# Kernel optimization log

Measured on AMD Instinct MI355X. Metric: run time of the kernel, lower is better.

Reference implementation:

```python
import jax, jax.numpy as jnp
import numpy as np

N = 8192      # atoms
E = 4096      # edges (become transformer tokens)
E2 = 65536    # edges of second graph y
VOCAB = 119
DE = 200      # node_features == embedding_dim
D = 256
H = 8
L = 2
DFF = 2048


def _bn(x, g, b, eps=1e-6):
    m = x.mean(0)
    v = x.var(0)
    return (x - m) * jax.lax.rsqrt(v + eps) * g + b


def _ln(x, g, b, eps=1e-5):
    m = x.mean(-1, keepdims=True)
    v = ((x - m) ** 2).mean(-1, keepdims=True)
    return (x - m) * jax.lax.rsqrt(v + eps) * g + b


def _gcn(x, ei, W, b):
    # PyG GCNConv: add self loops, symmetric deg^-1/2 normalization
    n = x.shape[0]
    loop = jnp.arange(n)
    src = jnp.concatenate([ei[0], loop])
    dst = jnp.concatenate([ei[1], loop])
    deg = jax.ops.segment_sum(jnp.ones(src.shape[0], x.dtype), dst, num_segments=n)
    dinv = jnp.where(deg > 0, jax.lax.rsqrt(jnp.maximum(deg, 1e-12)), 0.0)
    msg = (x @ W)[src] * (dinv[src] * dinv[dst])[:, None]
    return jax.ops.segment_sum(msg, dst, num_segments=n) + b


def _mha(x, wi, bi, wo, bo):
    S, d = x.shape
    dh = d // H
    q, k, v = jnp.split(x @ wi + bi, 3, axis=1)
    q = q.reshape(S, H, dh)
    k = k.reshape(S, H, dh)
    v = v.reshape(S, H, dh)
    sc = jnp.einsum('qhd,khd->hqk', q, k) * (1.0 / np.sqrt(dh))
    a = jax.nn.softmax(sc, axis=-1)
    o = jnp.einsum('hqk,khd->qhd', a, v).reshape(S, d)
    return o @ wo + bo


def setup_inputs() -> dict:
    key = jax.random.key(0)
    ks = iter(jax.random.split(key, 64))
    nrm = lambda shape, s=0.05: jax.random.normal(next(ks), shape, jnp.float32) * s
    d = {}
    d['x'] = jax.random.randint(next(ks), (N,), 0, VOCAB)
    d['edge_index'] = jax.random.randint(next(ks), (2, E), 1, N + 1)  # 1-based, code subtracts 1
    d['pos'] = jax.random.normal(next(ks), (N, 3), jnp.float32)
    d['y'] = jax.random.randint(next(ks), (2, E2), 0, E)
    d['emb'] = nrm((VOCAB, DE), 1.0)
    d['fc1_w'] = nrm((1, DE))
    d['fc1_b'] = jnp.zeros((DE,), jnp.float32)
    d['bn4_g'] = jnp.ones((DE,), jnp.float32)
    d['bn4_b'] = jnp.zeros((DE,), jnp.float32)
    d['conv1_w'] = nrm((DE, D))
    d['conv1_b'] = jnp.zeros((D,), jnp.float32)
    d['conv2_w'] = nrm((D, D))
    d['conv2_b'] = jnp.zeros((D,), jnp.float32)
    for i in (1, 2, 3):
        d['bn%d_g' % i] = jnp.ones((D,), jnp.float32)
        d['bn%d_b' % i] = jnp.zeros((D,), jnp.float32)
    d['in_proj_w'] = nrm((L, D, 3 * D))
    d['in_proj_b'] = jnp.zeros((L, 3 * D), jnp.float32)
    d['out_proj_w'] = nrm((L, D, D))
    d['out_proj_b'] = jnp.zeros((L, D), jnp.float32)
    d['ln1_g'] = jnp.ones((L, D), jnp.float32)
    d['ln1_b'] = jnp.zeros((L, D), jnp.float32)
    d['ln2_g'] = jnp.ones((L, D), jnp.float32)
    d['ln2_b'] = jnp.zeros((L, D), jnp.float32)
    d['ff1_w'] = nrm((L, D, DFF))
    d['ff1_b'] = jnp.zeros((L, DFF), jnp.float32)
    d['ff2_w'] = nrm((L, DFF, D))
    d['ff2_b'] = jnp.zeros((L, D), jnp.float32)
    d['fc3_w'] = nrm((D, 1))
    d['fc3_b'] = jnp.zeros((1,), jnp.float32)
    d['fc4_w'] = nrm((D, 9))
    d['fc4_b'] = jnp.zeros((9,), jnp.float32)
    return d


def reference(x, edge_index, pos, y, emb, fc1_w, fc1_b, bn4_g, bn4_b,
              conv1_w, conv1_b, conv2_w, conv2_b,
              bn1_g, bn1_b, bn2_g, bn2_b, bn3_g, bn3_b,
              in_proj_w, in_proj_b, out_proj_w, out_proj_b,
              ln1_g, ln1_b, ln2_g, ln2_b, ff1_w, ff1_b, ff2_w, ff2_b,
              fc3_w, fc3_b, fc4_w, fc4_b):
    h = emb[x]                                   # [N, DE]
    ei = edge_index - 1
    row, col = ei[0], ei[1]
    ef = jnp.linalg.norm(pos[col] - pos[row], axis=1, keepdims=True)  # [E,1]
    ef = _bn(ef @ fc1_w + fc1_b, bn4_g, bn4_b)   # [E, DE]
    h = h[row] + h[col] + ef                     # [E, DE] edges -> tokens
    h = jax.nn.leaky_relu(_gcn(h, y, conv1_w, conv1_b))
    h = _bn(h, bn1_g, bn1_b)
    h = jax.nn.leaky_relu(h + _gcn(h, y, conv2_w, conv2_b))
    h = _bn(h, bn2_g, bn2_b)
    # post-norm TransformerEncoder (unbatched seq of length E), dropout=0
    for i in range(L):
        h = _ln(h + _mha(h, in_proj_w[i], in_proj_b[i], out_proj_w[i], out_proj_b[i]),
                ln1_g[i], ln1_b[i])
        ff = jax.nn.relu(h @ ff1_w[i] + ff1_b[i]) @ ff2_w[i] + ff2_b[i]
        h = _ln(h + ff, ln2_g[i], ln2_b[i])
    h = jax.nn.leaky_relu(h)
    h = _bn(h, bn3_g, bn3_b)
    sym_out = h @ fc3_w + fc3_b
    asym_out = h @ fc4_w + fc4_b
    return (sym_out, asym_out)
```

## Files before the change

### kernel.cpp

```cpp
#include <hip/hip_runtime.h>
#include <math.h>

#define ETOK 4096
#define NE2  65536
#define DEF  200
#define DM   256
#define NH   8
#define DH   32
#define DFFN 2048
#define NKS  8

#define QSCALE_LOG2E 0.25503474f

typedef __attribute__((ext_vector_type(8))) short bfrag8;
typedef __attribute__((ext_vector_type(4))) float f32x4;
typedef __attribute__((ext_vector_type(4))) short short4v;
typedef __attribute__((ext_vector_type(4))) unsigned int u32x4;

__device__ __forceinline__ unsigned short f2bf(float f) {
  union { float f; unsigned u; } v; v.f = f;
  unsigned u = v.u + 0x7fffu + ((v.u >> 16) & 1u);
  return (unsigned short)(u >> 16);
}
__device__ __forceinline__ float bf2f(unsigned short u) {
  union { unsigned u; float f; } v;
  v.u = ((unsigned)u) << 16;
  return v.f;
}
__device__ __forceinline__ unsigned cvt_pk_bf16(float lo, float hi) {
  unsigned r;
  asm("v_cvt_pk_bf16_f32 %0, %1, %2" : "=v"(r) : "v"(lo), "v"(hi));
  return r;
}

__device__ __forceinline__ float wave_sum(float v) {
#pragma unroll
  for (int off = 32; off > 0; off >>= 1) v += __shfl_xor(v, off);
  return v;
}
__device__ __forceinline__ float block_sum(float v, float* red) {
  v = wave_sum(v);
  int lane = threadIdx.x & 63, w = threadIdx.x >> 6;
  if (lane == 0) red[w] = v;
  __syncthreads();
  float t = red[0] + red[1] + red[2] + red[3];
  __syncthreads();
  return t;
}

__global__ void edge_deg_kernel(const int* __restrict__ ei, const float* __restrict__ pos,
                                float* __restrict__ ef0, float* __restrict__ stats,
                                const int* __restrict__ y, int* __restrict__ deg) {
  __shared__ float red[4];
  int e2 = blockIdx.x * 256 + threadIdx.x;
  atomicAdd(&deg[y[NE2 + e2]], 1);
  if (blockIdx.x < 16) {
    int e = blockIdx.x * 256 + threadIdx.x;
    int r = ei[e] - 1;
    int c = ei[ETOK + e] - 1;
    float dx = pos[c * 3 + 0] - pos[r * 3 + 0];
    float dy = pos[c * 3 + 1] - pos[r * 3 + 1];
    float dz = pos[c * 3 + 2] - pos[r * 3 + 2];
    float d = sqrtf(dx * dx + dy * dy + dz * dz);
    ef0[e] = d;
    float s = block_sum(d, red);
    float s2 = block_sum(d * d, red);
    if (threadIdx.x == 0) {
      atomicAdd(stats + 0, s);
      atomicAdd(stats + 1, s2);
    }
  }
}

__global__ void token_build_kernel(const int* __restrict__ x, const int* __restrict__ ei,
                                   const float* __restrict__ emb, const float* __restrict__ fc1_w,
                                   const float* __restrict__ bn4_g, const float* __restrict__ bn4_b,
                                   const float* __restrict__ ef0, const float* __restrict__ stats,
                                   unsigned short* __restrict__ tokbf) {
  int e = blockIdx.x;
  int j = threadIdx.x;
  float m = stats[0] * (1.0f / 4096.0f);
  float v = stats[1] * (1.0f / 4096.0f) - m * m;
  int xr = x[ei[e] - 1];
  int xc = x[ei[ETOK + e] - 1];
  float dd = ef0[e] - m;
  float val = 0.f;
  if (j < DEF) {
    float w = fc1_w[j];
    float s = w * rsqrtf(v * w * w + 1e-6f) * bn4_g[j];
    val = emb[(size_t)xr * DEF + j] + emb[(size_t)xc * DEF + j] + dd * s + bn4_b[j];
  }
  tokbf[(size_t)e * 256 + j] = f2bf(val);
}

__global__ void scan_kernel(const int* __restrict__ deg, int* __restrict__ off,
                            int* __restrict__ cursor, float* __restrict__ dinv) {
  __shared__ int part[256];
  int t = threadIdx.x;
  int v[16];
  int s = 0;
#pragma unroll
  for (int i = 0; i < 16; ++i) {
    v[i] = deg[t * 16 + i];
    s += v[i];
  }
  part[t] = s;
  __syncthreads();
  if (t == 0) {
    int a = 0;
#pragma unroll 1
    for (int i = 0; i < 256; ++i) {
      int tmp = part[i];
      part[i] = a;
      a += tmp;
    }
    off[4096] = a;
  }
  __syncthreads();
  int a = part[t];
#pragma unroll
  for (int i = 0; i < 16; ++i) {
    off[t * 16 + i] = a;
    cursor[t * 16 + i] = a;
    dinv[t * 16 + i] = rsqrtf((float)(v[i] + 1));
    a += v[i];
  }
}
__global__ void fill_kernel(const int* __restrict__ y, int* __restrict__ cursor,
                            int* __restrict__ srcl) {
  int e = blockIdx.x * 256 + threadIdx.x;
  int s = y[e];
  int d = y[NE2 + e];
  int slot = atomicAdd(&cursor[d], 1);
  srcl[slot] = s;
}

template <int RES, int ACT>
__global__ __launch_bounds__(256) void gather_kernel(const float* __restrict__ xw,
                                                     const int* __restrict__ off,
                                                     const int* __restrict__ srcl,
                                                     const float* __restrict__ dinv,
                                                     const float* __restrict__ bias,
                                                     const float* __restrict__ resid,
                                                     float* __restrict__ out) {
  __shared__ int slds[256];
  __shared__ float dlds[256];
  const int d = blockIdx.x;
  const int c = threadIdx.x;
  const int b0 = off[d], b1 = off[d + 1];
  const float dd = dinv[d];
  float acc = 0.f;
  for (int base = b0; base < b1; base += 256) {
    int n = min(256, b1 - base);
    __syncthreads();
    if (c < n) {
      int s = srcl[base + c];
      slds[c] = s;
      dlds[c] = dinv[s];
    }
    __syncthreads();
    for (int j = 0; j < n; ++j) {
      int s = slds[j];
      acc = fmaf(xw[(size_t)s * DM + c], dlds[j], acc);
    }
  }
  size_t idx = (size_t)d * DM + c;
  float v = bias[c] + xw[idx] * dd * dd + acc * dd;
  if (RES) v += resid[idx];
  if (ACT) v = v > 0.f ? v : 0.01f * v;
  out[idx] = v;
}

struct WEntry {
  const float* src;
  unsigned short* dst;
  int K, N, KP, tilesN, ntiles;
};
struct WPack {
  WEntry e[10];
};
__global__ __launch_bounds__(256) void wtrans_all_kernel(WPack p) {
  __shared__ float tl[32][33];
  int t = blockIdx.x;
  int i = 0;
  while (t >= p.e[i].ntiles) {
    t -= p.e[i].ntiles;
    ++i;
  }
  const WEntry w = p.e[i];
  int nb = (t % w.tilesN) * 32;
  int kb = (t / w.tilesN) * 32;
  int tx = threadIdx.x & 31, ty = threadIdx.x >> 5;
#pragma unroll
  for (int r = ty; r < 32; r += 8) {
    int k = kb + r, n = nb + tx;
    tl[r][tx] = (k < w.K && n < w.N) ? w.src[(size_t)k * w.N + n] : 0.f;
  }
  __syncthreads();
#pragma unroll
  for (int r = ty; r < 32; r += 8) {
    int n = nb + r, k = kb + tx;
    if (n < w.N) w.dst[(size_t)n * w.KP + k] = f2bf(tl[tx][r]);
  }
}

template <int BM, int BN, int OUTBF, int ACT, int QS, int VSPLIT>
__global__ __launch_bounds__(256) void mfma_gemm(const unsigned short* __restrict__ A,
                                                 const unsigned short* __restrict__ Bt,
                                                 const float* __restrict__ bias,
                                                 void* __restrict__ Cout, void* __restrict__ Cout2,
                                                 int M, int N, int K) {
  constexpr int BK = 64;
  constexpr int TM = BM / 32, TN = BN / 32;
  constexpr int ACH = BM / 32, BCH = BN / 32;
  __shared__ unsigned short Alds[BM * BK];
  __shared__ unsigned short Blds[BN * BK];
  const int tid = threadIdx.x;
  const int lane = tid & 63, wid = tid >> 6;
  const int g = lane >> 4, q = lane & 15;
  const int wr = wid >> 1, wc = wid & 1;
  const int m0 = blockIdx.y * BM, n0 = blockIdx.x * BN;

  f32x4 acc[TM][TN];
#pragma unroll
  for (int i = 0; i < TM; ++i)
#pragma unroll
    for (int j = 0; j < TN; ++j) acc[i][j] = (f32x4){0.f, 0.f, 0.f, 0.f};

  for (int k0 = 0; k0 < K; k0 += BK) {
    __syncthreads();
#pragma unroll
    for (int c = 0; c < ACH; ++c) {
      int chunk = wid * ACH + c;
      int row = chunk * 8 + (lane >> 3);
      int cb = ((lane & 7) * 16) ^ ((row & 7) << 4);
      const char* gp = (const char*)A + ((size_t)(m0 + row) * K + k0) * 2 + cb;
      __builtin_amdgcn_global_load_lds(
          (const __attribute__((address_space(1))) unsigned int*)gp,
          (__attribute__((address_space(3))) unsigned int*)(Alds + chunk * 512), 16, 0, 0);
    }
#pragma unroll
    for (int c = 0; c < BCH; ++c) {
      int chunk = wid * BCH + c;
      int row = chunk * 8 + (lane >> 3);
      int cb = ((lane & 7) * 16) ^ ((row & 7) << 4);
      const char* gp = (const char*)Bt + ((size_t)(n0 + row) * K + k0) * 2 + cb;
      __builtin_amdgcn_global_load_lds(
          (const __attribute__((address_space(1))) unsigned int*)gp,
          (__attribute__((address_space(3))) unsigned int*)(Blds + chunk * 512), 16, 0, 0);
    }
    __syncthreads();
#pragma unroll
    for (int ks = 0; ks < 2; ++ks) {
      bfrag8 af[TM], bfr[TN];
#pragma unroll
      for (int mi = 0; mi < TM; ++mi) {
        int row = wr * (BM / 2) + mi * 16 + q;
        int cb = (ks * 64 + g * 16) ^ ((row & 7) << 4);
        af[mi] = *(const bfrag8*)((const char*)Alds + row * 128 + cb);
      }
#pragma unroll
      for (int ni = 0; ni < TN; ++ni) {
        int row = wc * (BN / 2) + ni * 16 + q;
        int cb = (ks * 64 + g * 16) ^ ((row & 7) << 4);
        bfr[ni] = *(const bfrag8*)((const char*)Blds + row * 128 + cb);
      }
#pragma unroll
      for (int mi = 0; mi < TM; ++mi)
#pragma unroll
        for (int ni = 0; ni < TN; ++ni)
          acc[mi][ni] = __builtin_amdgcn_mfma_f32_16x16x32_bf16(af[mi], bfr[ni], acc[mi][ni], 0, 0, 0);
    }
  }
#pragma unroll
  for (int mi = 0; mi < TM; ++mi) {
    int row = m0 + wr * (BM / 2) + mi * 16 + g * 4;
#pragma unroll
    for (int ni = 0; ni < TN; ++ni) {
      int col = n0 + wc * (BN / 2) + ni * 16 + q;
      float bv = bias ? bias[col] : 0.f;
      if (VSPLIT && col >= 512) {
        short4v pkv;
#pragma unroll
        for (int r = 0; r < 4; ++r) pkv[r] = (short)f2bf(acc[mi][ni][r] + bv);
        *(short4v*)((unsigned short*)Cout2 + (size_t)(col - 512) * M + row) = pkv;
      } else {
#pragma unroll
        for (int r = 0; r < 4; ++r) {
          float v = acc[mi][ni][r] + bv;
          if (QS && col < DM) v *= QSCALE_LOG2E;
          if (ACT == 1) v = fmaxf(v, 0.f);
          if (OUTBF)
            ((unsigned short*)Cout)[(size_t)(row + r) * (VSPLIT ? 512 : N) + col] = f2bf(v);
          else
            ((float*)Cout)[(size_t)(row + r) * N + col] = v;
        }
      }
    }
  }
}

template <int LEAKY>
__global__ __launch_bounds__(256) void col_accum_kernel(const float* __restrict__ x,
                                                        float* __restrict__ colm,
                                                        float* __restrict__ colv) {
  int c = threadIdx.x;
  int r0 = blockIdx.x * 16;
  float s = 0.f, s2 = 0.f;
#pragma unroll
  for (int i = 0; i < 16; ++i) {
    float v = x[(size_t)(r0 + i) * DM + c];
    if (LEAKY) v = v > 0.f ? v : 0.01f * v;
    s += v;
    s2 += v * v;
  }
  atomicAdd(&colm[c], s);
  atomicAdd(&colv[c], s2);
}
template <int LEAKY>
__global__ void bn_apply_kernel(const float* __restrict__ x, const float* __restrict__ colm,
                                const float* __restrict__ colv, const float* __restrict__ g,
                                const float* __restrict__ b, float* __restrict__ outf,
                                unsigned short* __restrict__ outb, int C) {
  size_t i = (size_t)blockIdx.x * 256 + threadIdx.x;
  int c = (int)(i % C);
  float mean = colm[c] * (1.0f / 4096.0f);
  float var = colv[c] * (1.0f / 4096.0f) - mean * mean;
  float v0 = x[i];
  if (LEAKY) v0 = v0 > 0.f ? v0 : 0.01f * v0;
  float v = (v0 - mean) * rsqrtf(var + 1e-6f) * g[c] + b[c];
  outf[i] = v;
  if (outb) outb[i] = f2bf(v);
}

__global__ __launch_bounds__(256, 6) void attn_mfma_kernel(const unsigned short* __restrict__ qk,
                                                           const unsigned short* __restrict__ vt,
                                                           unsigned short* __restrict__ Opart,
                                                           float* __restrict__ Lpart) {
  const int h = blockIdx.y;
  const int qblk = blockIdx.x * 128;
  const int chunk = blockIdx.z;
  const int tid = threadIdx.x;
  const int wid = tid >> 6, lane = tid & 63;
  const int g = lane >> 4, q = lane & 15;

  __shared__ unsigned short Klds[64][40];
  __shared__ unsigned int Vtw[32][36];
  __shared__ unsigned short Plds[4][32][40];

  bfrag8 qfrag0, qfrag1;
  {
    const unsigned short* qp = qk + (size_t)(qblk + wid * 32 + q) * 512 + h * DH + g * 8;
    qfrag0 = *(const bfrag8*)qp;
    qfrag1 = *(const bfrag8*)(qp + 16 * 512);
  }
  bfrag8 ones;
#pragma unroll
  for (int i = 0; i < 8; ++i) ones[i] = (short)0x3F80;
  const f32x4 zero = {0.f, 0.f, 0.f, 0.f};

  const int skey = tid >> 2;
  const int sdb = (tid & 3) * 8;
  const int sd = tid >> 3;
  const int sk4 = (tid & 7) * 4;

  const int kbeg = chunk * (ETOK / NKS);
  const int NT = (ETOK / NKS) / 64;

  const unsigned short* kptr = qk + (size_t)(kbeg + skey) * 512 + DM + h * DH + sdb;
  const unsigned short* vptr = vt + (size_t)(h * DH + sd) * ETOK + kbeg + sk4 * 2;

  bfrag8 kreg = *(const bfrag8*)kptr;
  kptr += (size_t)64 * 512;
  u32x4 vreg = *(const u32x4*)vptr;
  vptr += 64;

  f32x4 o00 = zero, o01 = zero, o10 = zero, o11 = zero;
  f32x4 ol0 = zero, ol1 = zero;

  for (int t = 0; t < NT; ++t) {
    *(bfrag8*)&Klds[skey][sdb] = kreg;
    *(u32x4*)&Vtw[sd][sk4] = vreg;
    __syncthreads();
    if (t + 1 < NT) {
      kreg = *(const bfrag8*)kptr;
      kptr += (size_t)64 * 512;
      vreg = *(const u32x4*)vptr;
      vptr += 64;
    }

#pragma unroll
    for (int kg = 0; kg < 2; ++kg) {
      f32x4 s0a, s0b, s1a, s1b;
      __builtin_amdgcn_s_setprio(1);
      {
        bfrag8 kfa = *(const bfrag8*)&Klds[(2 * kg) * 16 + q][g * 8];
        bfrag8 kfb = *(const bfrag8*)&Klds[(2 * kg + 1) * 16 + q][g * 8];
        s0a = __builtin_amdgcn_mfma_f32_16x16x32_bf16(kfa, qfrag0, zero, 0, 0, 0);
        s1a = __builtin_amdgcn_mfma_f32_16x16x32_bf16(kfa, qfrag1, zero, 0, 0, 0);
        s0b = __builtin_amdgcn_mfma_f32_16x16x32_bf16(kfb, qfrag0, zero, 0, 0, 0);
        s1b = __builtin_amdgcn_mfma_f32_16x16x32_bf16(kfb, qfrag1, zero, 0, 0, 0);
      }
      __builtin_amdgcn_s_setprio(0);

      {
        uint2 w2;
        w2.x = cvt_pk_bf16(__builtin_exp2f(s0a[0]), __builtin_exp2f(s0a[1]));
        w2.y = cvt_pk_bf16(__builtin_exp2f(s0a[2]), __builtin_exp2f(s0a[3]));
        *(uint2*)&Plds[wid][q][g * 4] = w2;
        w2.x = cvt_pk_bf16(__builtin_exp2f(s0b[0]), __builtin_exp2f(s0b[1]));
        w2.y = cvt_pk_bf16(__builtin_exp2f(s0b[2]), __builtin_exp2f(s0b[3]));
        *(uint2*)&Plds[wid][q][16 + g * 4] = w2;
        w2.x = cvt_pk_bf16(__builtin_exp2f(s1a[0]), __builtin_exp2f(s1a[1]));
        w2.y = cvt_pk_bf16(__builtin_exp2f(s1a[2]), __builtin_exp2f(s1a[3]));
        *(uint2*)&Plds[wid][16 + q][g * 4] = w2;
        w2.x = cvt_pk_bf16(__builtin_exp2f(s1b[0]), __builtin_exp2f(s1b[1]));
        w2.y = cvt_pk_bf16(__builtin_exp2f(s1b[2]), __builtin_exp2f(s1b[3]));
        *(uint2*)&Plds[wid][16 + q][16 + g * 4] = w2;
      }

      __builtin_amdgcn_s_setprio(1);
      {
        bfrag8 pa0 = *(const bfrag8*)&Plds[wid][q][g * 8];
        bfrag8 pa1 = *(const bfrag8*)&Plds[wid][16 + q][g * 8];
        bfrag8 vb0 = *(const bfrag8*)&Vtw[q][kg * 16 + g * 4];
        bfrag8 vb1 = *(const bfrag8*)&Vtw[16 + q][kg * 16 + g * 4];
        o00 = __builtin_amdgcn_mfma_f32_16x16x32_bf16(pa0, vb0, o00, 0, 0, 0);
        o01 = __builtin_amdgcn_mfma_f32_16x16x32_bf16(pa0, vb1, o01, 0, 0, 0);
        o10 = __builtin_amdgcn_mfma_f32_16x16x32_bf16(pa1, vb0, o10, 0, 0, 0);
        o11 = __builtin_amdgcn_mfma_f32_16x16x32_bf16(pa1, vb1, o11, 0, 0, 0);
        ol0 = __builtin_amdgcn_mfma_f32_16x16x32_bf16(pa0, ones, ol0, 0, 0, 0);
        ol1 = __builtin_amdgcn_mfma_f32_16x16x32_bf16(pa1, ones, ol1, 0, 0, 0);
      }
      __builtin_amdgcn_s_setprio(0);
    }
    __syncthreads();
  }

#pragma unroll
  for (int r = 0; r < 4; ++r) {
    int row0 = qblk + wid * 32 + g * 4 + r;
    unsigned short* op0 = Opart + ((size_t)chunk * ETOK + row0) * DM + h * DH;
    op0[q] = f2bf(o00[r]);
    op0[16 + q] = f2bf(o01[r]);
    unsigned short* op1 = op0 + (size_t)16 * DM;
    op1[q] = f2bf(o10[r]);
    op1[16 + q] = f2bf(o11[r]);
  }
  if (q == 0) {
#pragma unroll
    for (int r = 0; r < 4; ++r) {
      int row = qblk + wid * 32 + g * 4 + r;
      Lpart[((size_t)chunk * ETOK + row) * NH + h] = ol0[r];
      Lpart[((size_t)chunk * ETOK + row + 16) * NH + h] = ol1[r];
    }
  }
}

__global__ __launch_bounds__(256) void attn_combine_kernel(const unsigned short* __restrict__ Opart,
                                                           const float* __restrict__ Lpart,
                                                           unsigned short* __restrict__ out) {
  __shared__ float ls[NKS][NH];
  const int row = blockIdx.x;
  const int c = threadIdx.x;
  if (c < NKS * NH) {
    ls[c >> 3][c & 7] = Lpart[((size_t)(c >> 3) * ETOK + row) * NH + (c & 7)];
  }
  __syncthreads();
  const int h = c >> 5;
  float lstar = 0.f, acc = 0.f;
#pragma unroll
  for (int ch = 0; ch < NKS; ++ch) {
    lstar += ls[ch][h];
    acc += bf2f(Opart[((size_t)ch * ETOK + row) * DM + c]);
  }
  out[(size_t)row * DM + c] = f2bf(acc / lstar);
}

__global__ void add_ln_kernel(const float* __restrict__ x, const float* __restrict__ r,
                              float* __restrict__ outf, unsigned short* __restrict__ outb,
                              const float* __restrict__ g, const float* __restrict__ b) {
  __shared__ float red[4];
  int row = blockIdx.x, t = threadIdx.x;
  size_t idx = (size_t)row * DM + t;
  float v = x[idx] + r[idx];
  float mean = block_sum(v, red) * (1.0f / 256.0f);
  float dv = v - mean;
  float var = block_sum(dv * dv, red) * (1.0f / 256.0f);
  float o = dv * rsqrtf(var + 1e-5f) * g[t] + b[t];
  outf[idx] = o;
  outb[idx] = f2bf(o);
}

__global__ void head_kernel(const float* __restrict__ h, const float* __restrict__ colm,
                            const float* __restrict__ colv, const float* __restrict__ bng,
                            const float* __restrict__ bnb, const float* __restrict__ fc3w,
                            const float* __restrict__ fc3b, const float* __restrict__ fc4w,
                            const float* __restrict__ fc4b, float* __restrict__ out) {
  int wave = threadIdx.x >> 6, lane = threadIdx.x & 63;
  int tok = blockIdx.x * 4 + wave;
  const float* hr = h + (size_t)tok * DM;
  float hv[4];
#pragma unroll
  for (int i = 0; i < 4; ++i) {
    int col = lane * 4 + i;
    float v = hr[col];
    v = v > 0.f ? v : 0.01f * v;
    float mean = colm[col] * (1.0f / 4096.0f);
    float var = colv[col] * (1.0f / 4096.0f) - mean * mean;
    hv[i] = (v - mean) * rsqrtf(var + 1e-6f) * bng[col] + bnb[col];
  }
  float acc = 0.f;
#pragma unroll
  for (int i = 0; i < 4; ++i) acc += hv[i] * fc3w[lane * 4 + i];
  acc = wave_sum(acc);
  if (lane == 0) out[tok] = acc + fc3b[0];
#pragma unroll
  for (int j = 0; j < 9; ++j) {
    float a = 0.f;
#pragma unroll
    for (int i = 0; i < 4; ++i) a += hv[i] * fc4w[(lane * 4 + i) * 9 + j];
    a = wave_sum(a);
    if (lane == 0) out[ETOK + (size_t)tok * 9 + j] = a + fc4b[j];
  }
}

extern "C" void kernel_launch(void* const* d_in, const int* in_sizes, int n_in,
                              void* d_out, int out_size, void* d_ws, size_t ws_size,
                              hipStream_t stream) {
  const int* x = (const int*)d_in[0];
  const int* edge_index = (const int*)d_in[1];
  const float* pos = (const float*)d_in[2];
  const int* y = (const int*)d_in[3];
  const float* emb = (const float*)d_in[4];
  const float* fc1_w = (const float*)d_in[5];
  const float* bn4_g = (const float*)d_in[7];
  const float* bn4_b = (const float*)d_in[8];
  const float* conv1_w = (const float*)d_in[9];
  const float* conv1_b = (const float*)d_in[10];
  const float* conv2_w = (const float*)d_in[11];
  const float* conv2_b = (const float*)d_in[12];
  const float* bn1_g = (const float*)d_in[13];
  const float* bn1_b = (const float*)d_in[14];
  const float* bn2_g = (const float*)d_in[15];
  const float* bn2_b = (const float*)d_in[16];
  const float* bn3_g = (const float*)d_in[17];
  const float* bn3_b = (const float*)d_in[18];
  const float* ipw = (const float*)d_in[19];
  const float* ipb = (const float*)d_in[20];
  const float* opw = (const float*)d_in[21];
  const float* opb = (const float*)d_in[22];
  const float* ln1_g = (const float*)d_in[23];
  const float* ln1_b = (const float*)d_in[24];
  const float* ln2_g = (const float*)d_in[25];
  const float* ln2_b = (const float*)d_in[26];
  const float* ff1w = (const float*)d_in[27];
  const float* ff1b = (const float*)d_in[28];
  const float* ff2w = (const float*)d_in[29];
  const float* ff2b = (const float*)d_in[30];
  const float* fc3w = (const float*)d_in[31];
  const float* fc3b = (const float*)d_in[32];
  const float* fc4w = (const float*)d_in[33];
  const float* fc4b = (const float*)d_in[34];
  float* outp = (float*)d_out;

  char* wsp = (char*)d_ws;
  auto alloc = [&](size_t bytes) {
    void* p = (void*)wsp;
    wsp += (bytes + 255) & ~(size_t)255;
    return p;
  };
  unsigned short* big_bf = (unsigned short*)alloc((size_t)ETOK * DFFN * 2);
  unsigned short* qk_bf = (unsigned short*)alloc((size_t)ETOK * 512 * 2);
  unsigned short* vt_bf = (unsigned short*)alloc((size_t)DM * ETOK * 2);
  unsigned short* attno = (unsigned short*)alloc((size_t)ETOK * DM * 2);
  unsigned short* h_bf = (unsigned short*)alloc((size_t)ETOK * DM * 2);
  unsigned short* tok_bf = (unsigned short*)alloc((size_t)ETOK * 256 * 2);
  float* hf = (float*)alloc((size_t)ETOK * DM * 4);
  float* t1 = (float*)alloc((size_t)ETOK * DM * 4);
  float* t2 = (float*)alloc((size_t)ETOK * DM * 4);
  unsigned short* Opart = (unsigned short*)alloc((size_t)NKS * ETOK * DM * 2);
  float* Lpart = (float*)alloc((size_t)NKS * ETOK * NH * 4);
  unsigned short* c1wt = (unsigned short*)alloc(256 * 256 * 2);
  unsigned short* c2wt = (unsigned short*)alloc(256 * 256 * 2);
  unsigned short* ipwt = (unsigned short*)alloc((size_t)2 * 768 * 256 * 2);
  unsigned short* opwt = (unsigned short*)alloc((size_t)2 * 256 * 256 * 2);
  unsigned short* f1wt = (unsigned short*)alloc((size_t)2 * 2048 * 256 * 2);
  unsigned short* f2wt = (unsigned short*)alloc((size_t)2 * 256 * 2048 * 2);
  float* ef0 = (float*)alloc(ETOK * 4);
  float* dinv = (float*)alloc(ETOK * 4);
  int* off = (int*)alloc((ETOK + 1) * 4);
  int* cursor = (int*)alloc(ETOK * 4);
  int* srcl = (int*)alloc(NE2 * 4);
  char* z0 = wsp;
  float* stats = (float*)alloc(8 * 4);
  float* colm = (float*)alloc(3 * DM * 4);
  float* colv = (float*)alloc(3 * DM * 4);
  int* deg = (int*)alloc(ETOK * 4);
  size_t zlen = (char*)wsp - z0;

  hipMemsetAsync(z0, 0, zlen, stream);

  WPack wp;
  int ntot = 0;
  auto went = [&](int i, const float* src, unsigned short* dst, int K, int N, int KP) {
    wp.e[i].src = src;
    wp.e[i].dst = dst;
    wp.e[i].K = K;
    wp.e[i].N = N;
    wp.e[i].KP = KP;
    wp.e[i].tilesN = (N + 31) / 32;
    wp.e[i].ntiles = ((N + 31) / 32) * (KP / 32);
    ntot += wp.e[i].ntiles;
  };
  went(0, conv1_w, c1wt, 200, 256, 256);
  went(1, conv2_w, c2wt, 256, 256, 256);
  went(2, ipw, ipwt, 256, 768, 256);
  went(3, ipw + (size_t)256 * 768, ipwt + (size_t)768 * 256, 256, 768, 256);
  went(4, opw, opwt, 256, 256, 256);
  went(5, opw + (size_t)256 * 256, opwt + (size_t)256 * 256, 256, 256, 256);
  went(6, ff1w, f1wt, 256, 2048, 256);
  went(7, ff1w + (size_t)256 * 2048, f1wt + (size_t)2048 * 256, 256, 2048, 256);
  went(8, ff2w, f2wt, 2048, 256, 2048);
  went(9, ff2w + (size_t)2048 * 256, f2wt + (size_t)256 * 2048, 2048, 256, 2048);
  wtrans_all_kernel<<<ntot, 256, 0, stream>>>(wp);

  edge_deg_kernel<<<NE2 / 256, 256, 0, stream>>>(edge_index, pos, ef0, stats, y, deg);
  scan_kernel<<<1, 256, 0, stream>>>(deg, off, cursor, dinv);
  fill_kernel<<<NE2 / 256, 256, 0, stream>>>(y, cursor, srcl);
  token_build_kernel<<<ETOK, 256, 0, stream>>>(x, edge_index, emb, fc1_w, bn4_g, bn4_b, ef0,
                                               stats, tok_bf);

  mfma_gemm<32, 32, 0, 0, 0, 0><<<dim3(8, 128), 256, 0, stream>>>(tok_bf, c1wt, nullptr, t1,
                                                                  nullptr, ETOK, DM, 256);
  gather_kernel<0, 1><<<ETOK, 256, 0, stream>>>(t1, off, srcl, dinv, conv1_b, nullptr, t2);
  col_accum_kernel<0><<<ETOK / 16, 256, 0, stream>>>(t2, colm, colv);
  bn_apply_kernel<0><<<ETOK * DM / 256, 256, 0, stream>>>(t2, colm, colv, bn1_g, bn1_b, hf, h_bf, DM);

  mfma_gemm<32, 32, 0, 0, 0, 0><<<dim3(8, 128), 256, 0, stream>>>(h_bf, c2wt, nullptr, t1,
                                                                  nullptr, ETOK, DM, 256);
  gather_kernel<1, 1><<<ETOK, 256, 0, stream>>>(t1, off, srcl, dinv, conv2_b, hf, t2);
  col_accum_kernel<0><<<ETOK / 16, 256, 0, stream>>>(t2, colm + DM, colv + DM);
  bn_apply_kernel<0><<<ETOK * DM / 256, 256, 0, stream>>>(t2, colm + DM, colv + DM, bn2_g, bn2_b,
                                                          hf, h_bf, DM);

  for (int i = 0; i < 2; ++i) {
    mfma_gemm<32, 32, 1, 0, 1, 1><<<dim3(24, 128), 256, 0, stream>>>(
        h_bf, ipwt + (size_t)i * 768 * 256, ipb + (size_t)i * 768, qk_bf, vt_bf, ETOK, 768, 256);
    attn_mfma_kernel<<<dim3(ETOK / 128, NH, NKS), 256, 0, stream>>>(qk_bf, vt_bf, Opart, Lpart);
    attn_combine_kernel<<<ETOK, 256, 0, stream>>>(Opart, Lpart, attno);
    mfma_gemm<32, 32, 0, 0, 0, 0><<<dim3(8, 128), 256, 0, stream>>>(
        attno, opwt + (size_t)i * 256 * 256, opb + (size_t)i * DM, t2, nullptr, ETOK, DM, 256);
    add_ln_kernel<<<ETOK, 256, 0, stream>>>(t2, hf, hf, h_bf, ln1_g + (size_t)i * DM,
                                            ln1_b + (size_t)i * DM);
    mfma_gemm<64, 64, 1, 1, 0, 0><<<dim3(32, 64), 256, 0, stream>>>(
        h_bf, f1wt + (size_t)i * 2048 * 256, ff1b + (size_t)i * DFFN, big_bf, nullptr, ETOK, DFFN, 256);
    mfma_gemm<32, 32, 0, 0, 0, 0><<<dim3(8, 128), 256, 0, stream>>>(
        big_bf, f2wt + (size_t)i * 256 * 2048, ff2b + (size_t)i * DM, t2, nullptr, ETOK, DM, 2048);
    add_ln_kernel<<<ETOK, 256, 0, stream>>>(t2, hf, hf, h_bf, ln2_g + (size_t)i * DM,
                                            ln2_b + (size_t)i * DM);
  }

  col_accum_kernel<1><<<ETOK / 16, 256, 0, stream>>>(hf, colm + 2 * DM, colv + 2 * DM);
  head_kernel<<<ETOK / 4, 256, 0, stream>>>(hf, colm + 2 * DM, colv + 2 * DM, bn3_g, bn3_b,
                                            fc3w, fc3b, fc4w, fc4b, outp);
}
```

Before: 321.7 us.

## Keep attention P in registers via transposed MFMA and permuted V layout

The attention kernel now computes S^T per 16-row query fragment and feeds the exponentiated scores directly from registers as the B operand of the PV MFMA. This removes the per-wave P round trip through LDS. To make the register layout line up, the QKV GEMM writes V^T with a permuted row order, and the output and row-sum stores are rewritten to match. Separately, several GEMM launches switch from 32x32 to 64x32 tiles, halving the grid size, which trades parallelism for more reuse per block.

```diff
diff --git a/kernel.cpp b/kernel.cpp
--- a/kernel.cpp
+++ b/kernel.cpp
@@ -280,10 +280,11 @@
       int col = n0 + wc * (BN / 2) + ni * 16 + q;
       float bv = bias ? bias[col] : 0.f;
       if (VSPLIT && col >= 512) {
+        int prow = (row & ~31) | (((row >> 2) & 3) << 3) | (((row >> 4) & 1) << 2);
         short4v pkv;
 #pragma unroll
         for (int r = 0; r < 4; ++r) pkv[r] = (short)f2bf(acc[mi][ni][r] + bv);
-        *(short4v*)((unsigned short*)Cout2 + (size_t)(col - 512) * M + row) = pkv;
+        *(short4v*)((unsigned short*)Cout2 + (size_t)(col - 512) * M + prow) = pkv;
       } else {
 #pragma unroll
         for (int r = 0; r < 4; ++r) {
@@ -346,7 +347,6 @@
 
   __shared__ unsigned short Klds[64][40];
   __shared__ unsigned int Vtw[32][36];
-  __shared__ unsigned short Plds[4][32][40];
 
   bfrag8 qfrag0, qfrag1;
   {
@@ -390,47 +390,44 @@
     }
 
 #pragma unroll
-    for (int kg = 0; kg < 2; ++kg) {
-      f32x4 s0a, s0b, s1a, s1b;
+    for (int qf = 0; qf < 2; ++qf) {
+      bfrag8 qq = qf ? qfrag1 : qfrag0;
+      f32x4 st[4];
       __builtin_amdgcn_s_setprio(1);
-      {
-        bfrag8 kfa = *(const bfrag8*)&Klds[(2 * kg) * 16 + q][g * 8];
-        bfrag8 kfb = *(const bfrag8*)&Klds[(2 * kg + 1) * 16 + q][g * 8];
-        s0a = __builtin_amdgcn_mfma_f32_16x16x32_bf16(kfa, qfrag0, zero, 0, 0, 0);
-        s1a = __builtin_amdgcn_mfma_f32_16x16x32_bf16(kfa, qfrag1, zero, 0, 0, 0);
-        s0b = __builtin_amdgcn_mfma_f32_16x16x32_bf16(kfb, qfrag0, zero, 0, 0, 0);
-        s1b = __builtin_amdgcn_mfma_f32_16x16x32_bf16(kfb, qfrag1, zero, 0, 0, 0);
+#pragma unroll
+      for (int tt = 0; tt < 4; ++tt) {
+        bfrag8 kf = *(const bfrag8*)&Klds[tt * 16 + q][g * 8];
+        st[tt] = __builtin_amdgcn_mfma_f32_16x16x32_bf16(kf, qq, zero, 0, 0, 0);
       }
       __builtin_amdgcn_s_setprio(0);
 
-      {
-        uint2 w2;
-        w2.x = cvt_pk_bf16(__builtin_exp2f(s0a[0]), __builtin_exp2f(s0a[1]));
-        w2.y = cvt_pk_bf16(__builtin_exp2f(s0a[2]), __builtin_exp2f(s0a[3]));
-        *(uint2*)&Plds[wid][q][g * 4] = w2;
-        w2.x = cvt_pk_bf16(__builtin_exp2f(s0b[0]), __builtin_exp2f(s0b[1]));
-        w2.y = cvt_pk_bf16(__builtin_exp2f(s0b[2]), __builtin_exp2f(s0b[3]));
-        *(uint2*)&Plds[wid][q][16 + g * 4] = w2;
-        w2.x = cvt_pk_bf16(__builtin_exp2f(s1a[0]), __builtin_exp2f(s1a[1]));
-        w2.y = cvt_pk_bf16(__builtin_exp2f(s1a[2]), __builtin_exp2f(s1a[3]));
-        *(uint2*)&Plds[wid][16 + q][g * 4] = w2;
-        w2.x = cvt_pk_bf16(__builtin_exp2f(s1b[0]), __builtin_exp2f(s1b[1]));
-        w2.y = cvt_pk_bf16(__builtin_exp2f(s1b[2]), __builtin_exp2f(s1b[3]));
-        *(uint2*)&Plds[wid][16 + q][16 + g * 4] = w2;
-      }
+      u32x4 pwa, pwb;
+      pwa[0] = cvt_pk_bf16(__builtin_exp2f(st[0][0]), __builtin_exp2f(st[0][1]));
+      pwa[1] = cvt_pk_bf16(__builtin_exp2f(st[0][2]), __builtin_exp2f(st[0][3]));
+      pwa[2] = cvt_pk_bf16(__builtin_exp2f(st[1][0]), __builtin_exp2f(st[1][1]));
+      pwa[3] = cvt_pk_bf16(__builtin_exp2f(st[1][2]), __builtin_exp2f(st[1][3]));
+      pwb[0] = cvt_pk_bf16(__builtin_exp2f(st[2][0]), __builtin_exp2f(st[2][1]));
+      pwb[1] = cvt_pk_bf16(__builtin_exp2f(st[2][2]), __builtin_exp2f(st[2][3]));
+      pwb[2] = cvt_pk_bf16(__builtin_exp2f(st[3][0]), __builtin_exp2f(st[3][1]));
+      pwb[3] = cvt_pk_bf16(__builtin_exp2f(st[3][2]), __builtin_exp2f(st[3][3]));
+      bfrag8 pf0 = __builtin_bit_cast(bfrag8, pwa);
+      bfrag8 pf1 = __builtin_bit_cast(bfrag8, pwb);
 
       __builtin_amdgcn_s_setprio(1);
-      {
-        bfrag8 pa0 = *(const bfrag8*)&Plds[wid][q][g * 8];
-        bfrag8 pa1 = *(const bfrag8*)&Plds[wid][16 + q][g * 8];
-        bfrag8 vb0 = *(const bfrag8*)&Vtw[q][kg * 16 + g * 4];
-        bfrag8 vb1 = *(const bfrag8*)&Vtw[16 + q][kg * 16 + g * 4];
-        o00 = __builtin_amdgcn_mfma_f32_16x16x32_bf16(pa0, vb0, o00, 0, 0, 0);
-        o01 = __builtin_amdgcn_mfma_f32_16x16x32_bf16(pa0, vb1, o01, 0, 0, 0);
-        o10 = __builtin_amdgcn_mfma_f32_16x16x32_bf16(pa1, vb0, o10, 0, 0, 0);
-        o11 = __builtin_amdgcn_mfma_f32_16x16x32_bf16(pa1, vb1, o11, 0, 0, 0);
-        ol0 = __builtin_amdgcn_mfma_f32_16x16x32_bf16(pa0, ones, ol0, 0, 0, 0);
-        ol1 = __builtin_amdgcn_mfma_f32_16x16x32_bf16(pa1, ones, ol1, 0, 0, 0);
+#pragma unroll
+      for (int kg = 0; kg < 2; ++kg) {
+        bfrag8 pf = kg ? pf1 : pf0;
+        bfrag8 vf0 = *(const bfrag8*)&Vtw[q][kg * 16 + g * 4];
+        bfrag8 vf1 = *(const bfrag8*)&Vtw[16 + q][kg * 16 + g * 4];
+        if (qf == 0) {
+          o00 = __builtin_amdgcn_mfma_f32_16x16x32_bf16(vf0, pf, o00, 0, 0, 0);
+          o01 = __builtin_amdgcn_mfma_f32_16x16x32_bf16(vf1, pf, o01, 0, 0, 0);
+          ol0 = __builtin_amdgcn_mfma_f32_16x16x32_bf16(ones, pf, ol0, 0, 0, 0);
+        } else {
+          o10 = __builtin_amdgcn_mfma_f32_16x16x32_bf16(vf0, pf, o10, 0, 0, 0);
+          o11 = __builtin_amdgcn_mfma_f32_16x16x32_bf16(vf1, pf, o11, 0, 0, 0);
+          ol1 = __builtin_amdgcn_mfma_f32_16x16x32_bf16(ones, pf, ol1, 0, 0, 0);
+        }
       }
       __builtin_amdgcn_s_setprio(0);
     }
@@ -438,22 +435,22 @@
   }
 
 #pragma unroll
-  for (int r = 0; r < 4; ++r) {
-    int row0 = qblk + wid * 32 + g * 4 + r;
-    unsigned short* op0 = Opart + ((size_t)chunk * ETOK + row0) * DM + h * DH;
-    op0[q] = f2bf(o00[r]);
-    op0[16 + q] = f2bf(o01[r]);
-    unsigned short* op1 = op0 + (size_t)16 * DM;
-    op1[q] = f2bf(o10[r]);
-    op1[16 + q] = f2bf(o11[r]);
-  }
-  if (q == 0) {
-#pragma unroll
-    for (int r = 0; r < 4; ++r) {
-      int row = qblk + wid * 32 + g * 4 + r;
-      Lpart[((size_t)chunk * ETOK + row) * NH + h] = ol0[r];
-      Lpart[((size_t)chunk * ETOK + row + 16) * NH + h] = ol1[r];
-    }
+  for (int qf = 0; qf < 2; ++qf) {
+    int qrow = qblk + wid * 32 + qf * 16 + q;
+    unsigned short* op = Opart + ((size_t)chunk * ETOK + qrow) * DM + h * DH;
+#pragma unroll
+    for (int dblk = 0; dblk < 2; ++dblk) {
+      f32x4 ov = qf ? (dblk ? o11 : o10) : (dblk ? o01 : o00);
+      short4v pk;
+#pragma unroll
+      for (int r = 0; r < 4; ++r) pk[r] = (short)f2bf(ov[r]);
+      *(short4v*)(op + dblk * 16 + g * 4) = pk;
+    }
+  }
+  if (lane < 16) {
+    int row0 = qblk + wid * 32 + lane;
+    Lpart[((size_t)chunk * ETOK + row0) * NH + h] = ol0[0];
+    Lpart[((size_t)chunk * ETOK + row0 + 16) * NH + h] = ol1[0];
   }
 }
 
@@ -631,31 +628,31 @@
   token_build_kernel<<<ETOK, 256, 0, stream>>>(x, edge_index, emb, fc1_w, bn4_g, bn4_b, ef0,
                                                stats, tok_bf);
 
-  mfma_gemm<32, 32, 0, 0, 0, 0><<<dim3(8, 128), 256, 0, stream>>>(tok_bf, c1wt, nullptr, t1,
-                                                                  nullptr, ETOK, DM, 256);
+  mfma_gemm<64, 32, 0, 0, 0, 0><<<dim3(8, 64), 256, 0, stream>>>(tok_bf, c1wt, nullptr, t1,
+                                                                 nullptr, ETOK, DM, 256);
   gather_kernel<0, 1><<<ETOK, 256, 0, stream>>>(t1, off, srcl, dinv, conv1_b, nullptr, t2);
   col_accum_kernel<0><<<ETOK / 16, 256, 0, stream>>>(t2, colm, colv);
   bn_apply_kernel<0><<<ETOK * DM / 256, 256, 0, stream>>>(t2, colm, colv, bn1_g, bn1_b, hf, h_bf, DM);
 
-  mfma_gemm<32, 32, 0, 0, 0, 0><<<dim3(8, 128), 256, 0, stream>>>(h_bf, c2wt, nullptr, t1,
-                                                                  nullptr, ETOK, DM, 256);
+  mfma_gemm<64, 32, 0, 0, 0, 0><<<dim3(8, 64), 256, 0, stream>>>(h_bf, c2wt, nullptr, t1,
+                                                                 nullptr, ETOK, DM, 256);
   gather_kernel<1, 1><<<ETOK, 256, 0, stream>>>(t1, off, srcl, dinv, conv2_b, hf, t2);
   col_accum_kernel<0><<<ETOK / 16, 256, 0, stream>>>(t2, colm + DM, colv + DM);
   bn_apply_kernel<0><<<ETOK * DM / 256, 256, 0, stream>>>(t2, colm + DM, colv + DM, bn2_g, bn2_b,
                                                           hf, h_bf, DM);
 
   for (int i = 0; i < 2; ++i) {
-    mfma_gemm<32, 32, 1, 0, 1, 1><<<dim3(24, 128), 256, 0, stream>>>(
+    mfma_gemm<64, 32, 1, 0, 1, 1><<<dim3(24, 64), 256, 0, stream>>>(
         h_bf, ipwt + (size_t)i * 768 * 256, ipb + (size_t)i * 768, qk_bf, vt_bf, ETOK, 768, 256);
     attn_mfma_kernel<<<dim3(ETOK / 128, NH, NKS), 256, 0, stream>>>(qk_bf, vt_bf, Opart, Lpart);
     attn_combine_kernel<<<ETOK, 256, 0, stream>>>(Opart, Lpart, attno);
-    mfma_gemm<32, 32, 0, 0, 0, 0><<<dim3(8, 128), 256, 0, stream>>>(
+    mfma_gemm<64, 32, 0, 0, 0, 0><<<dim3(8, 64), 256, 0, stream>>>(
         attno, opwt + (size_t)i * 256 * 256, opb + (size_t)i * DM, t2, nullptr, ETOK, DM, 256);
     add_ln_kernel<<<ETOK, 256, 0, stream>>>(t2, hf, hf, h_bf, ln1_g + (size_t)i * DM,
                                             ln1_b + (size_t)i * DM);
     mfma_gemm<64, 64, 1, 1, 0, 0><<<dim3(32, 64), 256, 0, stream>>>(
         h_bf, f1wt + (size_t)i * 2048 * 256, ff1b + (size_t)i * DFFN, big_bf, nullptr, ETOK, DFFN, 256);
-    mfma_gemm<32, 32, 0, 0, 0, 0><<<dim3(8, 128), 256, 0, stream>>>(
+    mfma_gemm<64, 32, 0, 0, 0, 0><<<dim3(8, 64), 256, 0, stream>>>(
         big_bf, f2wt + (size_t)i * 256 * 2048, ff2b + (size_t)i * DM, t2, nullptr, ETOK, DM, 2048);
     add_ln_kernel<<<ETOK, 256, 0, stream>>>(t2, hf, hf, h_bf, ln2_g + (size_t)i * DM,
                                             ln2_b + (size_t)i * DM);
```

Result: slower. 386.2 us (+20.1%).
